# Kernel optimization log

Measured on AMD Instinct MI355X. Metric: run time of the kernel, lower is better.

The kernel has to match this reference:

```python
import jax, jax.numpy as jnp
from jax import lax
import numpy as np

N, L, C, G, K = 8, 4096, 256, 8, 3
GC = C // G
DILATION = 1
OFFSET_SCALE = 1.0
LN_EPS = 1e-6


def setup_inputs() -> dict:
    key = jax.random.key(0)
    ks = jax.random.split(key, 14)
    s = lambda k, shp, sc: jax.random.normal(k, shp, jnp.float32) * sc
    return {
        "x": jax.random.normal(ks[0], (N, L, C), jnp.float32),
        "W_in": s(ks[1], (C, C), (1.0 / C) ** 0.5),      # input_proj (in,out)
        "b_in": jnp.zeros((C,), jnp.float32),
        "conv_w": s(ks[2], (C, 1, K), 0.2),              # depthwise conv (O, I/g, K)
        "conv_b": jnp.zeros((C,), jnp.float32),
        "ln_g": jnp.ones((C,), jnp.float32),
        "ln_b": jnp.zeros((C,), jnp.float32),
        "W_off": s(ks[3], (C, G * K), 0.02),             # offset_linear
        "b_off": s(ks[4], (G * K,), 0.02),
        "W_mask": s(ks[5], (C, G * K), 0.02),            # mask_linear
        "b_mask": s(ks[6], (G * K,), 0.02),
        "W_out": s(ks[7], (C, C), (1.0 / C) ** 0.5),     # output_proj
        "b_out": jnp.zeros((C,), jnp.float32),
    }


def _dcnv3_1d(x, W_in, b_in, conv_w, conv_b, ln_g, ln_b,
              W_off, b_off, W_mask, b_mask, W_out, b_out):
    # x: (N, L, C)
    x_proj = x @ W_in + b_in                                     # (N,L,C)

    # depthwise conv -> LayerNorm(C) -> GELU  (the offset/mask feature branch)
    xc = x.transpose(0, 2, 1)                                    # (N,C,L)
    pad = (K - 1) // 2
    y = lax.conv_general_dilated(
        xc, conv_w, window_strides=(1,), padding=[(pad, pad)],
        dimension_numbers=("NCH", "OIH", "NCH"), feature_group_count=C)
    y = y + conv_b[None, :, None]
    y = y.transpose(0, 2, 1)                                     # (N,L,C)
    mu = y.mean(-1, keepdims=True)
    var = ((y - mu) ** 2).mean(-1, keepdims=True)
    y = (y - mu) * lax.rsqrt(var + LN_EPS) * ln_g + ln_b
    x_feat = jax.nn.gelu(y, approximate=False)                   # torch GELU = exact erf

    offset = (x_feat @ W_off + b_off).reshape(N, L, G, K)
    mask = jax.nn.softmax((x_feat @ W_mask + b_mask).reshape(N, L, G, K), axis=-1)

    # sampling locations (grid_sample with align_corners=True unnormalizes back to loc)
    ref_p = jnp.arange(L, dtype=jnp.float32)                     # (L,)
    lo = float(-((K - 1) // 2))
    hi = float((K - 1) // 2)
    dil_grid = jnp.linspace(lo, hi, K) * DILATION                # (K,)
    loc = ref_p[None, :, None, None] + dil_grid[None, None, None, :] \
          + offset * OFFSET_SCALE                                # (N,L,G,K)
    loc = jnp.remainder(loc, L)                                  # in [0, L)

    # bilinear sample along L with zero padding (matches F.grid_sample, H=1)
    f0 = jnp.floor(loc)
    w1 = loc - f0
    w0 = 1.0 - w1
    i0 = jnp.clip(f0.astype(jnp.int32), 0, L - 1)
    i1 = i0 + 1
    valid1 = (i1 < L)
    i1c = jnp.where(valid1, i1, 0)

    x_g = x_proj.reshape(N, L, G, GC)                            # (N,L,G,gc)
    nidx = jnp.arange(N)[:, None, None, None]
    gidx = jnp.arange(G)[None, None, :, None]
    v0 = x_g[nidx, i0, gidx]                                     # (N,L,G,K,gc)
    v1 = x_g[nidx, i1c, gidx] * valid1[..., None].astype(x_g.dtype)
    sampled = w0[..., None] * v0 + w1[..., None] * v1            # (N,L,G,K,gc)

    out = (sampled * mask[..., None]).sum(axis=3)                # (N,L,G,gc)
    out = out.reshape(N, L, C)
    return out @ W_out + b_out


def reference(x, W_in, b_in, conv_w, conv_b, ln_g, ln_b,
              W_off, b_off, W_mask, b_mask, W_out, b_out):
    return _dcnv3_1d(x, W_in, b_in, conv_w, conv_b, ln_g, ln_b,
                     W_off, b_off, W_mask, b_mask, W_out, b_out)
```

## Files before the change

kernel.cpp:

```cpp
#include <hip/hip_runtime.h>
#include <math.h>

constexpr int LL = 4096;
constexpr int CC = 256;
constexpr int MM = 32768;

typedef unsigned int u32;
typedef unsigned short u16;
typedef __attribute__((ext_vector_type(8))) short bf16x8;
typedef __attribute__((ext_vector_type(4))) float f32x4;

__device__ __forceinline__ u16 f2b(float f) {
    u32 u = __float_as_uint(f);
    u32 r = (u + 0x7fffu + ((u >> 16) & 1u)) >> 16;
    return (u16)r;
}
__device__ __forceinline__ u32 pack2(float a, float b) {
    return (u32)f2b(a) | ((u32)f2b(b) << 16);
}

__device__ __forceinline__ void gl_lds16(const u16* g, u16* l) {
    __builtin_amdgcn_global_load_lds(
        (const __attribute__((address_space(1))) unsigned int*)g,
        (__attribute__((address_space(3))) unsigned int*)l, 16, 0, 0);
}

__global__ __launch_bounds__(256) void conv_prep(
    const float* __restrict__ x, const float* __restrict__ cw,
    const float* __restrict__ cbias, const float* __restrict__ lng,
    const float* __restrict__ lnb, u16* __restrict__ xf,
    const float* __restrict__ W_in, const float* __restrict__ W_out,
    const float* __restrict__ W_off, const float* __restrict__ W_mask,
    u16* __restrict__ Wt_in, u16* __restrict__ Wt_out, u16* __restrict__ Wcomb)
{
    const int bid = blockIdx.x;
    const int t = threadIdx.x;
    if (bid >= 8192) {
        const int b = bid - 8192;
        if (b < 256) {
            Wt_in[b * 256 + t]  = f2b(W_in[t * 256 + b]);
            Wt_out[b * 256 + t] = f2b(W_out[t * 256 + b]);
        } else {
            const int j = b - 256;
            const float v = (j < 24) ? W_off[t * 24 + j] : W_mask[t * 24 + (j - 24)];
            Wcomb[j * 256 + t] = f2b(v);
        }
        return;
    }

    const int wave = t >> 6;
    const int lane = t & 63;
    const int nl = (bid << 2) + wave;
    const int l = nl & (LL - 1);
    const int c0 = lane << 2;
    const size_t base = (size_t)nl * CC + c0;

    float4 xc = *(const float4*)&x[base];
    float4 xm = make_float4(0.f, 0.f, 0.f, 0.f);
    float4 xp = make_float4(0.f, 0.f, 0.f, 0.f);
    if (l > 0)      xm = *(const float4*)&x[base - CC];
    if (l < LL - 1) xp = *(const float4*)&x[base + CC];

    float xmv[4] = {xm.x, xm.y, xm.z, xm.w};
    float xcv[4] = {xc.x, xc.y, xc.z, xc.w};
    float xpv[4] = {xp.x, xp.y, xp.z, xp.w};

    float y[4];
    float sum = 0.f, sq = 0.f;
#pragma unroll
    for (int j = 0; j < 4; ++j) {
        const int c = c0 + j;
        float v = fmaf(xmv[j], cw[c * 3 + 0],
                  fmaf(xcv[j], cw[c * 3 + 1],
                  fmaf(xpv[j], cw[c * 3 + 2], cbias[c])));
        y[j] = v;
        sum += v;
        sq  += v * v;
    }
#pragma unroll
    for (int off = 32; off > 0; off >>= 1) {
        sum += __shfl_xor(sum, off);
        sq  += __shfl_xor(sq, off);
    }
    const float mu  = sum * (1.f / CC);
    const float var = sq * (1.f / CC) - mu * mu;
    const float rs  = rsqrtf(var + 1e-6f);

    ushort4 o;
    float ov[4];
#pragma unroll
    for (int j = 0; j < 4; ++j) {
        const int c = c0 + j;
        const float tn = (y[j] - mu) * rs * lng[c] + lnb[c];
        ov[j] = 0.5f * tn * (1.f + erff(tn * 0.70710678118654752f));
    }
    o.x = f2b(ov[0]); o.y = f2b(ov[1]); o.z = f2b(ov[2]); o.w = f2b(ov[3]);
    *(ushort4*)&xf[base] = o;
}

__global__ __launch_bounds__(256, 2) void gemm1(
    const float* __restrict__ x, const u16* __restrict__ Wt_in,
    const float* __restrict__ b_in, u16* __restrict__ xprojb)
{
    __shared__ u16 As[2][128 * 32];
    __shared__ u16 Bs[2][128 * 32];

    const int t = threadIdx.x;
    const int w = t >> 6, lane = t & 63;
    const int lr = lane & 15, lk = lane >> 4;
    const int wm = w >> 1, wn = w & 1;

    const int d = blockIdx.x;
    const int m_t = (d & 7) * 32 + (d >> 4);
    const int n_t = (d >> 3) & 1;
    const int m0 = m_t * 128, n0 = n_t * 128;

    const int srow = lane >> 2;
    const int scol = (lane & 3) * 8;
    const int arow = t >> 1;
    const int akh = (t & 1) * 16;

    f32x4 acc[4][4];
#pragma unroll
    for (int i = 0; i < 4; ++i)
#pragma unroll
        for (int j = 0; j < 4; ++j) acc[i][j] = f32x4{0.f, 0.f, 0.f, 0.f};

    auto STAGE_B = [&](int buf, int kt) {
        const int k0 = kt * 32;
#pragma unroll
        for (int j = 0; j < 2; ++j) {
            const int rr = (w * 2 + j) * 16 + srow;
            gl_lds16(Wt_in + ((size_t)(n0 + rr) << 8) + k0 + scol,
                     &Bs[buf][0] + (w * 2 + j) * 512);
        }
    };
    const float* Abase = x + (size_t)(m0 + arow) * 256 + akh;

    {
        float4 f0 = *(const float4*)(Abase);
        float4 f1 = *(const float4*)(Abase + 4);
        float4 f2 = *(const float4*)(Abase + 8);
        float4 f3 = *(const float4*)(Abase + 12);
        STAGE_B(0, 0);
        u16* dst = &As[0][arow * 32 + akh];
        ((u32*)dst)[0] = pack2(f0.x, f0.y); ((u32*)dst)[1] = pack2(f0.z, f0.w);
        ((u32*)dst)[2] = pack2(f1.x, f1.y); ((u32*)dst)[3] = pack2(f1.z, f1.w);
        ((u32*)dst)[4] = pack2(f2.x, f2.y); ((u32*)dst)[5] = pack2(f2.z, f2.w);
        ((u32*)dst)[6] = pack2(f3.x, f3.y); ((u32*)dst)[7] = pack2(f3.z, f3.w);
    }

#pragma unroll
    for (int kt = 0; kt < 8; ++kt) {
        const int cur = kt & 1;
        __syncthreads();
        float4 f0, f1, f2, f3;
        if (kt < 7) {
            const float* ap = Abase + (kt + 1) * 32;
            f0 = *(const float4*)(ap);
            f1 = *(const float4*)(ap + 4);
            f2 = *(const float4*)(ap + 8);
            f3 = *(const float4*)(ap + 12);
            STAGE_B(cur ^ 1, kt + 1);
        }
        bf16x8 af[4], bfr[4];
#pragma unroll
        for (int mt = 0; mt < 4; ++mt)
            af[mt] = *(const bf16x8*)&As[cur][(wm * 64 + mt * 16 + lr) * 32 + lk * 8];
#pragma unroll
        for (int nt = 0; nt < 4; ++nt)
            bfr[nt] = *(const bf16x8*)&Bs[cur][(wn * 64 + nt * 16 + lr) * 32 + lk * 8];
#pragma unroll
        for (int mt = 0; mt < 4; ++mt)
#pragma unroll
            for (int nt = 0; nt < 4; ++nt)
                acc[mt][nt] = __builtin_amdgcn_mfma_f32_16x16x32_bf16(
                    af[mt], bfr[nt], acc[mt][nt], 0, 0, 0);
        if (kt < 7) {
            u16* dst = &As[cur ^ 1][arow * 32 + akh];
            ((u32*)dst)[0] = pack2(f0.x, f0.y); ((u32*)dst)[1] = pack2(f0.z, f0.w);
            ((u32*)dst)[2] = pack2(f1.x, f1.y); ((u32*)dst)[3] = pack2(f1.z, f1.w);
            ((u32*)dst)[4] = pack2(f2.x, f2.y); ((u32*)dst)[5] = pack2(f2.z, f2.w);
            ((u32*)dst)[6] = pack2(f3.x, f3.y); ((u32*)dst)[7] = pack2(f3.z, f3.w);
        }
    }

    const int r0 = lk * 4;
#pragma unroll
    for (int nt = 0; nt < 4; ++nt) {
        const int cn = n0 + wn * 64 + nt * 16 + lr;
        const float bv = b_in[cn];
#pragma unroll
        for (int mt = 0; mt < 4; ++mt)
#pragma unroll
            for (int r4 = 0; r4 < 4; ++r4)
                xprojb[(size_t)(m0 + wm * 64 + mt * 16 + r0 + r4) * 256 + cn] =
                    f2b(acc[mt][nt][r4] + bv);
    }
}

__global__ __launch_bounds__(256, 3) void offmask_gemm(
    const u16* __restrict__ xfeatb, const u16* __restrict__ xprojb,
    const u16* __restrict__ Wcomb, const float* __restrict__ boff,
    const float* __restrict__ bmask, const u16* __restrict__ Wt_out,
    const float* __restrict__ b_out, float* __restrict__ out)
{
    __shared__ __align__(16) char s_mem[32768];
    __shared__ uint2 s_pack[512 * 3];
    float* logit = (float*)s_mem;

    const int t = threadIdx.x;
    const int w = t >> 6, lane = t & 63;
    const int lr = lane & 15, lk8 = (lane >> 4) * 8;
    const int r0 = (lane >> 4) * 4;
    const int blk = blockIdx.x;
    const size_t row0 = (size_t)blk * 64;

    f32x4 pacc[3];
#pragma unroll
    for (int ct = 0; ct < 3; ++ct) pacc[ct] = f32x4{0.f, 0.f, 0.f, 0.f};
    const u16* fbase = xfeatb + (row0 + w * 16 + lr) * 256;
#pragma unroll
    for (int ks = 0; ks < 8; ++ks) {
        const int ke = ks * 32 + lk8;
        bf16x8 a = *(const bf16x8*)(fbase + ke);
#pragma unroll
        for (int ct = 0; ct < 3; ++ct) {
            bf16x8 bfr = *(const bf16x8*)(Wcomb + (size_t)(ct * 16 + lr) * 256 + ke);
            pacc[ct] = __builtin_amdgcn_mfma_f32_16x16x32_bf16(a, bfr, pacc[ct], 0, 0, 0);
        }
    }
#pragma unroll
    for (int ct = 0; ct < 3; ++ct) {
        const int j = ct * 16 + lr;
        const float bj = (j < 24) ? boff[j] : bmask[j - 24];
#pragma unroll
        for (int r4 = 0; r4 < 4; ++r4)
            logit[(w * 16 + r0 + r4) * 50 + j] = pacc[ct][r4] + bj;
    }
    __syncthreads();

#pragma unroll
    for (int pi = 0; pi < 2; ++pi) {
        const int pp = pi * 256 + t;
        const int rw = pp >> 3, g = pp & 7;
        const float* lp = &logit[rw * 50];
        const float m0v = lp[24 + g * 3 + 0];
        const float m1v = lp[24 + g * 3 + 1];
        const float m2v = lp[24 + g * 3 + 2];
        const float mx = fmaxf(m0v, fmaxf(m1v, m2v));
        const float e0 = expf(m0v - mx), e1 = expf(m1v - mx), e2 = expf(m2v - mx);
        const float inv = 1.f / (e0 + e1 + e2);
        const float msk[3] = {e0 * inv, e1 * inv, e2 * inv};
        const float lf = (float)((blk & 63) * 64 + rw);
#pragma unroll
        for (int k = 0; k < 3; ++k) {
            const float loc = lf + (float)(k - 1) + lp[g * 3 + k];
            float r = fmodf(loc, (float)LL);
            if (r < 0.f) r += (float)LL;
            const float f0 = floorf(r);
            int i0 = (int)f0;
            i0 = i0 < 0 ? 0 : (i0 > LL - 1 ? LL - 1 : i0);
            const int i1 = i0 + 1;
            const float w1 = r - f0;
            const bool valid = (i1 < LL);
            union { u32 uw; _Float16 h[2]; } uh;
            uh.h[0] = (_Float16)(msk[k] * (1.f - w1));
            uh.h[1] = (_Float16)(valid ? msk[k] * w1 : 0.f);
            const u32 ij = (u32)i0 | ((u32)(valid ? i1 : 0) << 16);
            s_pack[pp * 3 + k] = make_uint2(uh.uw, ij);
        }
    }
    __syncthreads();

    {
        const int ig = t >> 5, tc = t & 31;
        const int c0 = tc * 8, g4 = tc >> 2;
        const u16* xpn = xprojb + (size_t)(blk >> 6) * LL * 256;
        const int ibeg = ig * 8;
#pragma unroll 2
        for (int i = ibeg; i < ibeg + 8; ++i) {
            const int bidx = (i * 8 + g4) * 3;
            float v[8] = {0.f, 0.f, 0.f, 0.f, 0.f, 0.f, 0.f, 0.f};
#pragma unroll
            for (int k = 0; k < 3; ++k) {
                const uint2 pk = s_pack[bidx + k];
                union { u32 uw; _Float16 h[2]; } uh; uh.uw = pk.x;
                const float wa = (float)uh.h[0], wb = (float)uh.h[1];
                const int i0 = (int)(pk.y & 0xffffu), i1 = (int)(pk.y >> 16);
                uint4 ua = *(const uint4*)(xpn + (size_t)i0 * 256 + c0);
                uint4 ub = *(const uint4*)(xpn + (size_t)i1 * 256 + c0);
                const u32 au[4] = {ua.x, ua.y, ua.z, ua.w};
                const u32 bu[4] = {ub.x, ub.y, ub.z, ub.w};
#pragma unroll
                for (int j = 0; j < 4; ++j) {
                    v[2 * j]     = fmaf(wa, __uint_as_float(au[j] << 16),
                                   fmaf(wb, __uint_as_float(bu[j] << 16), v[2 * j]));
                    v[2 * j + 1] = fmaf(wa, __uint_as_float(au[j] & 0xffff0000u),
                                   fmaf(wb, __uint_as_float(bu[j] & 0xffff0000u), v[2 * j + 1]));
                }
            }
            uint4 wd;
            wd.x = pack2(v[0], v[1]); wd.y = pack2(v[2], v[3]);
            wd.z = pack2(v[4], v[5]); wd.w = pack2(v[6], v[7]);
            const int addr = (i * 512 + tc * 16) ^ ((i & 7) << 4);
            *(uint4*)(s_mem + addr) = wd;
        }
    }
    __syncthreads();

    f32x4 acc[4][4];
#pragma unroll
    for (int i = 0; i < 4; ++i)
#pragma unroll
        for (int j = 0; j < 4; ++j) acc[i][j] = f32x4{0.f, 0.f, 0.f, 0.f};

    const u16* Bw = Wt_out + (size_t)(w * 64) * 256;
#pragma unroll
    for (int ks = 0; ks < 8; ++ks) {
        bf16x8 af[4], bfr[4];
#pragma unroll
        for (int mt = 0; mt < 4; ++mt) {
            const int rm = mt * 16 + lr;
            const int addr = (rm * 512 + ks * 64 + lk8 * 2) ^ ((rm & 7) << 4);
            af[mt] = *(const bf16x8*)(s_mem + addr);
        }
        const int ke = ks * 32 + lk8;
#pragma unroll
        for (int nt = 0; nt < 4; ++nt)
            bfr[nt] = *(const bf16x8*)(Bw + (size_t)(nt * 16 + lr) * 256 + ke);
#pragma unroll
        for (int mt = 0; mt < 4; ++mt)
#pragma unroll
            for (int nt = 0; nt < 4; ++nt)
                acc[mt][nt] = __builtin_amdgcn_mfma_f32_16x16x32_bf16(
                    af[mt], bfr[nt], acc[mt][nt], 0, 0, 0);
    }
#pragma unroll
    for (int nt = 0; nt < 4; ++nt) {
        const int cn = w * 64 + nt * 16 + lr;
        const float bv = b_out[cn];
#pragma unroll
        for (int mt = 0; mt < 4; ++mt)
#pragma unroll
            for (int r4 = 0; r4 < 4; ++r4)
                out[(row0 + mt * 16 + r0 + r4) * 256 + cn] = acc[mt][nt][r4] + bv;
    }
}

extern "C" void kernel_launch(void* const* d_in, const int* in_sizes, int n_in,
                              void* d_out, int out_size, void* d_ws, size_t ws_size,
                              hipStream_t stream)
{
    const float* x      = (const float*)d_in[0];
    const float* W_in   = (const float*)d_in[1];
    const float* b_in   = (const float*)d_in[2];
    const float* conv_w = (const float*)d_in[3];
    const float* conv_b = (const float*)d_in[4];
    const float* ln_g   = (const float*)d_in[5];
    const float* ln_b   = (const float*)d_in[6];
    const float* W_off  = (const float*)d_in[7];
    const float* b_off  = (const float*)d_in[8];
    const float* W_mask = (const float*)d_in[9];
    const float* b_mask = (const float*)d_in[10];
    const float* W_out  = (const float*)d_in[11];
    const float* b_out  = (const float*)d_in[12];

    u16* xfeatb = (u16*)d_ws;
    u16* xprojb = (u16*)((char*)d_ws + 16777216);
    char* wsb   = (char*)d_ws + 33554432;
    u16* Wt_in  = (u16*)(wsb);
    u16* Wt_out = (u16*)(wsb + 131072);
    u16* Wcombp = (u16*)(wsb + 262144);

    conv_prep<<<8192 + 304, 256, 0, stream>>>(x, conv_w, conv_b, ln_g, ln_b, xfeatb,
                                              W_in, W_out, W_off, W_mask,
                                              Wt_in, Wt_out, Wcombp);
    gemm1<<<512, 256, 0, stream>>>(x, Wt_in, b_in, xprojb);
    offmask_gemm<<<512, 256, 0, stream>>>(xfeatb, xprojb, Wcombp, b_off, b_mask,
                                          Wt_out, b_out, (float*)d_out);
}
```

Measured before the change: 72.04 us.

## Split offset/mask projection into own kernel and shrink gather-GEMM tiles

The fused offmask_gemm kernel is split in two. A new proj_soft kernel computes offset/mask logits, the softmax and the sampling records, and writes them to a global workspace buffer. A gather_gemm kernel then reads those records, gathers from x_proj and runs the output projection over 32-row tiles, giving 1024 blocks at higher occupancy. conv_prep now handles two rows per wave, reusing the neighbouring loads and hoisting the per-channel weight loads. The split adds an extra kernel launch and a global round-trip for the sampling records.

```diff
diff --git a/kernel.cpp b/kernel.cpp
--- a/kernel.cpp
+++ b/kernel.cpp
@@ -35,8 +35,8 @@
 {
     const int bid = blockIdx.x;
     const int t = threadIdx.x;
-    if (bid >= 8192) {
-        const int b = bid - 8192;
+    if (bid >= 4096) {
+        const int b = bid - 4096;
         if (b < 256) {
             Wt_in[b * 256 + t]  = f2b(W_in[t * 256 + b]);
             Wt_out[b * 256 + t] = f2b(W_out[t * 256 + b]);
@@ -50,164 +50,70 @@
 
     const int wave = t >> 6;
     const int lane = t & 63;
-    const int nl = (bid << 2) + wave;
-    const int l = nl & (LL - 1);
+    const int nl0 = (bid << 3) + wave * 2;
+    const int l0 = nl0 & (LL - 1);
     const int c0 = lane << 2;
-    const size_t base = (size_t)nl * CC + c0;
-
-    float4 xc = *(const float4*)&x[base];
-    float4 xm = make_float4(0.f, 0.f, 0.f, 0.f);
-    float4 xp = make_float4(0.f, 0.f, 0.f, 0.f);
-    if (l > 0)      xm = *(const float4*)&x[base - CC];
-    if (l < LL - 1) xp = *(const float4*)&x[base + CC];
-
-    float xmv[4] = {xm.x, xm.y, xm.z, xm.w};
-    float xcv[4] = {xc.x, xc.y, xc.z, xc.w};
-    float xpv[4] = {xp.x, xp.y, xp.z, xp.w};
-
-    float y[4];
-    float sum = 0.f, sq = 0.f;
+    const size_t base = (size_t)nl0 * CC + c0;
+
+    const float4 zero = make_float4(0.f, 0.f, 0.f, 0.f);
+    float4 xm = (l0 > 0) ? *(const float4*)&x[base - CC] : zero;
+    float4 xa = *(const float4*)&x[base];
+    float4 xb = *(const float4*)&x[base + CC];
+    float4 xp = (l0 < LL - 2) ? *(const float4*)&x[base + 2 * CC] : zero;
+
+    const float cw0[4] = {cw[(c0+0)*3+0], cw[(c0+1)*3+0], cw[(c0+2)*3+0], cw[(c0+3)*3+0]};
+    const float cw1[4] = {cw[(c0+0)*3+1], cw[(c0+1)*3+1], cw[(c0+2)*3+1], cw[(c0+3)*3+1]};
+    const float cw2[4] = {cw[(c0+0)*3+2], cw[(c0+1)*3+2], cw[(c0+2)*3+2], cw[(c0+3)*3+2]};
+    const float cb4[4] = {cbias[c0+0], cbias[c0+1], cbias[c0+2], cbias[c0+3]};
+    const float lg4[4] = {lng[c0+0], lng[c0+1], lng[c0+2], lng[c0+3]};
+    const float lb4[4] = {lnb[c0+0], lnb[c0+1], lnb[c0+2], lnb[c0+3]};
+
+    const float pA[4] = {xm.x, xm.y, xm.z, xm.w};
+    const float cA[4] = {xa.x, xa.y, xa.z, xa.w};
+    const float nA[4] = {xb.x, xb.y, xb.z, xb.w};
+    const float nB[4] = {xp.x, xp.y, xp.z, xp.w};
+
+    float yA[4], yB[4];
+    float sA = 0.f, qA = 0.f, sB = 0.f, qB = 0.f;
 #pragma unroll
     for (int j = 0; j < 4; ++j) {
-        const int c = c0 + j;
-        float v = fmaf(xmv[j], cw[c * 3 + 0],
-                  fmaf(xcv[j], cw[c * 3 + 1],
-                  fmaf(xpv[j], cw[c * 3 + 2], cbias[c])));
-        y[j] = v;
-        sum += v;
-        sq  += v * v;
+        float vA = fmaf(pA[j], cw0[j], fmaf(cA[j], cw1[j], fmaf(nA[j], cw2[j], cb4[j])));
+        float vB = fmaf(cA[j], cw0[j], fmaf(nA[j], cw1[j], fmaf(nB[j], cw2[j], cb4[j])));
+        yA[j] = vA; sA += vA; qA += vA * vA;
+        yB[j] = vB; sB += vB; qB += vB * vB;
     }
 #pragma unroll
     for (int off = 32; off > 0; off >>= 1) {
-        sum += __shfl_xor(sum, off);
-        sq  += __shfl_xor(sq, off);
-    }
-    const float mu  = sum * (1.f / CC);
-    const float var = sq * (1.f / CC) - mu * mu;
-    const float rs  = rsqrtf(var + 1e-6f);
-
-    ushort4 o;
-    float ov[4];
+        sA += __shfl_xor(sA, off);
+        qA += __shfl_xor(qA, off);
+        sB += __shfl_xor(sB, off);
+        qB += __shfl_xor(qB, off);
+    }
+    const float muA = sA * (1.f / CC), muB = sB * (1.f / CC);
+    const float rsA = rsqrtf(qA * (1.f / CC) - muA * muA + 1e-6f);
+    const float rsB = rsqrtf(qB * (1.f / CC) - muB * muB + 1e-6f);
+
+    ushort4 oA, oB;
+    float vA[4], vB[4];
 #pragma unroll
     for (int j = 0; j < 4; ++j) {
-        const int c = c0 + j;
-        const float tn = (y[j] - mu) * rs * lng[c] + lnb[c];
-        ov[j] = 0.5f * tn * (1.f + erff(tn * 0.70710678118654752f));
-    }
-    o.x = f2b(ov[0]); o.y = f2b(ov[1]); o.z = f2b(ov[2]); o.w = f2b(ov[3]);
-    *(ushort4*)&xf[base] = o;
-}
-
-__global__ __launch_bounds__(256, 2) void gemm1(
-    const float* __restrict__ x, const u16* __restrict__ Wt_in,
-    const float* __restrict__ b_in, u16* __restrict__ xprojb)
+        const float tA = (yA[j] - muA) * rsA * lg4[j] + lb4[j];
+        const float tB = (yB[j] - muB) * rsB * lg4[j] + lb4[j];
+        vA[j] = 0.5f * tA * (1.f + erff(tA * 0.70710678118654752f));
+        vB[j] = 0.5f * tB * (1.f + erff(tB * 0.70710678118654752f));
+    }
+    oA.x = f2b(vA[0]); oA.y = f2b(vA[1]); oA.z = f2b(vA[2]); oA.w = f2b(vA[3]);
+    oB.x = f2b(vB[0]); oB.y = f2b(vB[1]); oB.z = f2b(vB[2]); oB.w = f2b(vB[3]);
+    *(ushort4*)&xf[base] = oA;
+    *(ushort4*)&xf[base + CC] = oB;
+}
+
+__global__ __launch_bounds__(256) void proj_soft(
+    const u16* __restrict__ xfeatb, const u16* __restrict__ Wcomb,
+    const float* __restrict__ boff, const float* __restrict__ bmask,
+    uint2* __restrict__ rec)
 {
-    __shared__ u16 As[2][128 * 32];
-    __shared__ u16 Bs[2][128 * 32];
-
-    const int t = threadIdx.x;
-    const int w = t >> 6, lane = t & 63;
-    const int lr = lane & 15, lk = lane >> 4;
-    const int wm = w >> 1, wn = w & 1;
-
-    const int d = blockIdx.x;
-    const int m_t = (d & 7) * 32 + (d >> 4);
-    const int n_t = (d >> 3) & 1;
-    const int m0 = m_t * 128, n0 = n_t * 128;
-
-    const int srow = lane >> 2;
-    const int scol = (lane & 3) * 8;
-    const int arow = t >> 1;
-    const int akh = (t & 1) * 16;
-
-    f32x4 acc[4][4];
-#pragma unroll
-    for (int i = 0; i < 4; ++i)
-#pragma unroll
-        for (int j = 0; j < 4; ++j) acc[i][j] = f32x4{0.f, 0.f, 0.f, 0.f};
-
-    auto STAGE_B = [&](int buf, int kt) {
-        const int k0 = kt * 32;
-#pragma unroll
-        for (int j = 0; j < 2; ++j) {
-            const int rr = (w * 2 + j) * 16 + srow;
-            gl_lds16(Wt_in + ((size_t)(n0 + rr) << 8) + k0 + scol,
-                     &Bs[buf][0] + (w * 2 + j) * 512);
-        }
-    };
-    const float* Abase = x + (size_t)(m0 + arow) * 256 + akh;
-
-    {
-        float4 f0 = *(const float4*)(Abase);
-        float4 f1 = *(const float4*)(Abase + 4);
-        float4 f2 = *(const float4*)(Abase + 8);
-        float4 f3 = *(const float4*)(Abase + 12);
-        STAGE_B(0, 0);
-        u16* dst = &As[0][arow * 32 + akh];
-        ((u32*)dst)[0] = pack2(f0.x, f0.y); ((u32*)dst)[1] = pack2(f0.z, f0.w);
-        ((u32*)dst)[2] = pack2(f1.x, f1.y); ((u32*)dst)[3] = pack2(f1.z, f1.w);
-        ((u32*)dst)[4] = pack2(f2.x, f2.y); ((u32*)dst)[5] = pack2(f2.z, f2.w);
-        ((u32*)dst)[6] = pack2(f3.x, f3.y); ((u32*)dst)[7] = pack2(f3.z, f3.w);
-    }
-
-#pragma unroll
-    for (int kt = 0; kt < 8; ++kt) {
-        const int cur = kt & 1;
-        __syncthreads();
-        float4 f0, f1, f2, f3;
-        if (kt < 7) {
-            const float* ap = Abase + (kt + 1) * 32;
-            f0 = *(const float4*)(ap);
-            f1 = *(const float4*)(ap + 4);
-            f2 = *(const float4*)(ap + 8);
-            f3 = *(const float4*)(ap + 12);
-            STAGE_B(cur ^ 1, kt + 1);
-        }
-        bf16x8 af[4], bfr[4];
-#pragma unroll
-        for (int mt = 0; mt < 4; ++mt)
-            af[mt] = *(const bf16x8*)&As[cur][(wm * 64 + mt * 16 + lr) * 32 + lk * 8];
-#pragma unroll
-        for (int nt = 0; nt < 4; ++nt)
-            bfr[nt] = *(const bf16x8*)&Bs[cur][(wn * 64 + nt * 16 + lr) * 32 + lk * 8];
-#pragma unroll
-        for (int mt = 0; mt < 4; ++mt)
-#pragma unroll
-            for (int nt = 0; nt < 4; ++nt)
-                acc[mt][nt] = __builtin_amdgcn_mfma_f32_16x16x32_bf16(
-                    af[mt], bfr[nt], acc[mt][nt], 0, 0, 0);
-        if (kt < 7) {
-            u16* dst = &As[cur ^ 1][arow * 32 + akh];
-            ((u32*)dst)[0] = pack2(f0.x, f0.y); ((u32*)dst)[1] = pack2(f0.z, f0.w);
-            ((u32*)dst)[2] = pack2(f1.x, f1.y); ((u32*)dst)[3] = pack2(f1.z, f1.w);
-            ((u32*)dst)[4] = pack2(f2.x, f2.y); ((u32*)dst)[5] = pack2(f2.z, f2.w);
-            ((u32*)dst)[6] = pack2(f3.x, f3.y); ((u32*)dst)[7] = pack2(f3.z, f3.w);
-        }
-    }
-
-    const int r0 = lk * 4;
-#pragma unroll
-    for (int nt = 0; nt < 4; ++nt) {
-        const int cn = n0 + wn * 64 + nt * 16 + lr;
-        const float bv = b_in[cn];
-#pragma unroll
-        for (int mt = 0; mt < 4; ++mt)
-#pragma unroll
-            for (int r4 = 0; r4 < 4; ++r4)
-                xprojb[(size_t)(m0 + wm * 64 + mt * 16 + r0 + r4) * 256 + cn] =
-                    f2b(acc[mt][nt][r4] + bv);
-    }
-}
-
-__global__ __launch_bounds__(256, 3) void offmask_gemm(
-    const u16* __restrict__ xfeatb, const u16* __restrict__ xprojb,
-    const u16* __restrict__ Wcomb, const float* __restrict__ boff,
-    const float* __restrict__ bmask, const u16* __restrict__ Wt_out,
-    const float* __restrict__ b_out, float* __restrict__ out)
-{
-    __shared__ __align__(16) char s_mem[32768];
-    __shared__ uint2 s_pack[512 * 3];
-    float* logit = (float*)s_mem;
+    __shared__ float logit[64 * 50];
 
     const int t = threadIdx.x;
     const int w = t >> 6, lane = t & 63;
@@ -253,6 +159,7 @@
         const float inv = 1.f / (e0 + e1 + e2);
         const float msk[3] = {e0 * inv, e1 * inv, e2 * inv};
         const float lf = (float)((blk & 63) * 64 + rw);
+        uint2* rbase = rec + row0 * 24 + pp * 3;
 #pragma unroll
         for (int k = 0; k < 3; ++k) {
             const float loc = lf + (float)(k - 1) + lp[g * 3 + k];
@@ -268,18 +175,141 @@
             uh.h[0] = (_Float16)(msk[k] * (1.f - w1));
             uh.h[1] = (_Float16)(valid ? msk[k] * w1 : 0.f);
             const u32 ij = (u32)i0 | ((u32)(valid ? i1 : 0) << 16);
-            s_pack[pp * 3 + k] = make_uint2(uh.uw, ij);
-        }
+            rbase[k] = make_uint2(uh.uw, ij);
+        }
+    }
+}
+
+__global__ __launch_bounds__(256, 2) void gemm1(
+    const float* __restrict__ x, const u16* __restrict__ Wt_in,
+    const float* __restrict__ b_in, u16* __restrict__ xprojb)
+{
+    __shared__ u16 As[2][128 * 32];
+    __shared__ u16 Bs[2][128 * 32];
+
+    const int t = threadIdx.x;
+    const int w = t >> 6, lane = t & 63;
+    const int lr = lane & 15, lk = lane >> 4;
+    const int wm = w >> 1, wn = w & 1;
+
+    const int d = blockIdx.x;
+    const int m_t = (d & 7) * 32 + (d >> 4);
+    const int n_t = (d >> 3) & 1;
+    const int m0 = m_t * 128, n0 = n_t * 128;
+
+    const int srow = lane >> 2;
+    const int scol = (lane & 3) * 8;
+    const int arow = t >> 1;
+    const int akh = (t & 1) * 16;
+
+    f32x4 acc[4][4];
+#pragma unroll
+    for (int i = 0; i < 4; ++i)
+#pragma unroll
+        for (int j = 0; j < 4; ++j) acc[i][j] = f32x4{0.f, 0.f, 0.f, 0.f};
+
+    auto STAGE_B = [&](int buf, int kt) {
+        const int k0 = kt * 32;
+#pragma unroll
+        for (int j = 0; j < 2; ++j) {
+            const int rr = (w * 2 + j) * 16 + srow;
+            gl_lds16(Wt_in + ((size_t)(n0 + rr) << 8) + k0 + scol,
+                     &Bs[buf][0] + (w * 2 + j) * 512);
+        }
+    };
+    const float* Abase = x + (size_t)(m0 + arow) * 256 + akh;
+
+    {
+        float4 f0 = *(const float4*)(Abase);
+        float4 f1 = *(const float4*)(Abase + 4);
+        float4 f2 = *(const float4*)(Abase + 8);
+        float4 f3 = *(const float4*)(Abase + 12);
+        STAGE_B(0, 0);
+        u16* dst = &As[0][arow * 32 + akh];
+        ((u32*)dst)[0] = pack2(f0.x, f0.y); ((u32*)dst)[1] = pack2(f0.z, f0.w);
+        ((u32*)dst)[2] = pack2(f1.x, f1.y); ((u32*)dst)[3] = pack2(f1.z, f1.w);
+        ((u32*)dst)[4] = pack2(f2.x, f2.y); ((u32*)dst)[5] = pack2(f2.z, f2.w);
+        ((u32*)dst)[6] = pack2(f3.x, f3.y); ((u32*)dst)[7] = pack2(f3.z, f3.w);
+    }
+
+#pragma unroll
+    for (int kt = 0; kt < 8; ++kt) {
+        const int cur = kt & 1;
+        __syncthreads();
+        float4 f0, f1, f2, f3;
+        if (kt < 7) {
+            const float* ap = Abase + (kt + 1) * 32;
+            f0 = *(const float4*)(ap);
+            f1 = *(const float4*)(ap + 4);
+            f2 = *(const float4*)(ap + 8);
+            f3 = *(const float4*)(ap + 12);
+            STAGE_B(cur ^ 1, kt + 1);
+        }
+        bf16x8 af[4], bfr[4];
+#pragma unroll
+        for (int mt = 0; mt < 4; ++mt)
+            af[mt] = *(const bf16x8*)&As[cur][(wm * 64 + mt * 16 + lr) * 32 + lk * 8];
+#pragma unroll
+        for (int nt = 0; nt < 4; ++nt)
+            bfr[nt] = *(const bf16x8*)&Bs[cur][(wn * 64 + nt * 16 + lr) * 32 + lk * 8];
+#pragma unroll
+        for (int mt = 0; mt < 4; ++mt)
+#pragma unroll
+            for (int nt = 0; nt < 4; ++nt)
+                acc[mt][nt] = __builtin_amdgcn_mfma_f32_16x16x32_bf16(
+                    af[mt], bfr[nt], acc[mt][nt], 0, 0, 0);
+        if (kt < 7) {
+            u16* dst = &As[cur ^ 1][arow * 32 + akh];
+            ((u32*)dst)[0] = pack2(f0.x, f0.y); ((u32*)dst)[1] = pack2(f0.z, f0.w);
+            ((u32*)dst)[2] = pack2(f1.x, f1.y); ((u32*)dst)[3] = pack2(f1.z, f1.w);
+            ((u32*)dst)[4] = pack2(f2.x, f2.y); ((u32*)dst)[5] = pack2(f2.z, f2.w);
+            ((u32*)dst)[6] = pack2(f3.x, f3.y); ((u32*)dst)[7] = pack2(f3.z, f3.w);
+        }
+    }
+
+    const int r0 = lk * 4;
+#pragma unroll
+    for (int nt = 0; nt < 4; ++nt) {
+        const int cn = n0 + wn * 64 + nt * 16 + lr;
+        const float bv = b_in[cn];
+#pragma unroll
+        for (int mt = 0; mt < 4; ++mt)
+#pragma unroll
+            for (int r4 = 0; r4 < 4; ++r4)
+                xprojb[(size_t)(m0 + wm * 64 + mt * 16 + r0 + r4) * 256 + cn] =
+                    f2b(acc[mt][nt][r4] + bv);
+    }
+}
+
+__global__ __launch_bounds__(256, 4) void gather_gemm(
+    const uint2* __restrict__ rec, const u16* __restrict__ xprojb,
+    const u16* __restrict__ Wt_out, const float* __restrict__ b_out,
+    float* __restrict__ out)
+{
+    __shared__ __align__(16) char s_mem[16384];
+    __shared__ uint2 s_pack[768];
+
+    const int t = threadIdx.x;
+    const int w = t >> 6, lane = t & 63;
+    const int lr = lane & 15, lk8 = (lane >> 4) * 8;
+    const int r0 = (lane >> 4) * 4;
+    const int blk = blockIdx.x;
+    const size_t row0 = (size_t)blk * 32;
+
+    {
+        const uint2* rb = rec + row0 * 24;
+#pragma unroll
+        for (int e = 0; e < 3; ++e) s_pack[t * 3 + e] = rb[t * 3 + e];
     }
     __syncthreads();
 
     {
         const int ig = t >> 5, tc = t & 31;
         const int c0 = tc * 8, g4 = tc >> 2;
-        const u16* xpn = xprojb + (size_t)(blk >> 6) * LL * 256;
-        const int ibeg = ig * 8;
-#pragma unroll 2
-        for (int i = ibeg; i < ibeg + 8; ++i) {
+        const u16* xpn = xprojb + (size_t)(blk >> 7) * LL * 256;
+        const int ibeg = ig * 4;
+#pragma unroll
+        for (int i = ibeg; i < ibeg + 4; ++i) {
             const int bidx = (i * 8 + g4) * 3;
             float v[8] = {0.f, 0.f, 0.f, 0.f, 0.f, 0.f, 0.f, 0.f};
 #pragma unroll
@@ -309,18 +339,18 @@
     }
     __syncthreads();
 
-    f32x4 acc[4][4];
-#pragma unroll
-    for (int i = 0; i < 4; ++i)
+    f32x4 acc[2][4];
+#pragma unroll
+    for (int i = 0; i < 2; ++i)
 #pragma unroll
         for (int j = 0; j < 4; ++j) acc[i][j] = f32x4{0.f, 0.f, 0.f, 0.f};
 
     const u16* Bw = Wt_out + (size_t)(w * 64) * 256;
 #pragma unroll
     for (int ks = 0; ks < 8; ++ks) {
-        bf16x8 af[4], bfr[4];
-#pragma unroll
-        for (int mt = 0; mt < 4; ++mt) {
+        bf16x8 af[2], bfr[4];
+#pragma unroll
+        for (int mt = 0; mt < 2; ++mt) {
             const int rm = mt * 16 + lr;
             const int addr = (rm * 512 + ks * 64 + lk8 * 2) ^ ((rm & 7) << 4);
             af[mt] = *(const bf16x8*)(s_mem + addr);
@@ -330,7 +360,7 @@
         for (int nt = 0; nt < 4; ++nt)
             bfr[nt] = *(const bf16x8*)(Bw + (size_t)(nt * 16 + lr) * 256 + ke);
 #pragma unroll
-        for (int mt = 0; mt < 4; ++mt)
+        for (int mt = 0; mt < 2; ++mt)
 #pragma unroll
             for (int nt = 0; nt < 4; ++nt)
                 acc[mt][nt] = __builtin_amdgcn_mfma_f32_16x16x32_bf16(
@@ -341,7 +371,7 @@
         const int cn = w * 64 + nt * 16 + lr;
         const float bv = b_out[cn];
 #pragma unroll
-        for (int mt = 0; mt < 4; ++mt)
+        for (int mt = 0; mt < 2; ++mt)
 #pragma unroll
             for (int r4 = 0; r4 < 4; ++r4)
                 out[(row0 + mt * 16 + r0 + r4) * 256 + cn] = acc[mt][nt][r4] + bv;
@@ -372,11 +402,12 @@
     u16* Wt_in  = (u16*)(wsb);
     u16* Wt_out = (u16*)(wsb + 131072);
     u16* Wcombp = (u16*)(wsb + 262144);
-
-    conv_prep<<<8192 + 304, 256, 0, stream>>>(x, conv_w, conv_b, ln_g, ln_b, xfeatb,
+    uint2* rec  = (uint2*)((char*)d_ws + 50331648);
+
+    conv_prep<<<4096 + 304, 256, 0, stream>>>(x, conv_w, conv_b, ln_g, ln_b, xfeatb,
                                               W_in, W_out, W_off, W_mask,
                                               Wt_in, Wt_out, Wcombp);
+    proj_soft<<<512, 256, 0, stream>>>(xfeatb, Wcombp, b_off, b_mask, rec);
     gemm1<<<512, 256, 0, stream>>>(x, Wt_in, b_in, xprojb);
-    offmask_gemm<<<512, 256, 0, stream>>>(xfeatb, xprojb, Wcombp, b_off, b_mask,
-                                          Wt_out, b_out, (float*)d_out);
-}
+    gather_gemm<<<1024, 256, 0, stream>>>(rec, xprojb, Wt_out, b_out, (float*)d_out);
+}
```

Result: no change. 72.34 us (+0.4%).
